# Optimization experiments

Hardware: AMD Instinct MI355X
Metric: run time of the kernel (lower is better)

## Reference

```python
import jax, jax.numpy as jnp
import numpy as np

NUM_HEADS = 16
HEAD_DIM = 64
HIDDEN = NUM_HEADS * HEAD_DIM  # 1024
B, T = 32, 512


def setup_inputs() -> dict:
    key = jax.random.key(0)
    ks = jax.random.split(key, 10)
    s = 1.0 / np.sqrt(HIDDEN)
    inp = {
        "x": jax.random.normal(ks[0], (B, HIDDEN, T), dtype=jnp.float32),
        "mask": jax.random.randint(ks[1], (B, T), 0, 2, dtype=jnp.int32),
        "Wq": jax.random.uniform(ks[2], (HIDDEN, HIDDEN), jnp.float32, -s, s),
        "bq": jax.random.uniform(ks[3], (HIDDEN,), jnp.float32, -s, s),
        "Wk": jax.random.uniform(ks[4], (HIDDEN, HIDDEN), jnp.float32, -s, s),
        "bk": jax.random.uniform(ks[5], (HIDDEN,), jnp.float32, -s, s),
        "Wv": jax.random.uniform(ks[6], (HIDDEN, HIDDEN), jnp.float32, -s, s),
        "bv": jax.random.uniform(ks[7], (HIDDEN,), jnp.float32, -s, s),
        "Wo": jax.random.uniform(ks[8], (HIDDEN, HIDDEN), jnp.float32, -s, s),
        "bo": jax.random.uniform(ks[9], (HIDDEN,), jnp.float32, -s, s),
    }
    return inp


def reference(x, mask, Wq, bq, Wk, bk, Wv, bv, Wo, bo):
    # x: [B, hidden, T] -> tokens along last axis
    b, h, t = x.shape
    xt = jnp.swapaxes(x, 1, 2)  # [B, T, hidden]

    def heads(w, bias):
        y = xt @ w.T + bias                       # [B, T, hidden]
        return y.reshape(b, t, NUM_HEADS, HEAD_DIM).transpose(0, 2, 1, 3)  # [B, nh, T, hd]

    q = heads(Wq, bq)
    k = heads(Wk, bk)
    v = heads(Wv, bv)

    scores = jnp.einsum("bhqd,bhkd->bhqk", q, k) / jnp.sqrt(jnp.float32(HEAD_DIM))
    # masked_fill(mask==0, -inf) then clamp to [-50, 50]: masked entries become -50
    scores = jnp.where(mask[:, None, None, :] == 0, -jnp.inf, scores)
    scores = jnp.clip(scores, -50.0, 50.0)
    attn = jax.nn.softmax(scores, axis=-1)        # [B, nh, T, T]
    out = jnp.einsum("bhqk,bhkd->bhqd", attn, v)  # [B, nh, T, hd]
    out = out.transpose(0, 2, 1, 3).reshape(b, t, h)
    out = out @ Wo.T + bo                         # [B, T, hidden]
    return out.max(axis=1)                        # [B, hidden]
```

## Files before the change

kernel.cpp:

```cpp
#include <hip/hip_runtime.h>


typedef _Float16 half8 __attribute__((ext_vector_type(8)));
typedef _Float16 half4 __attribute__((ext_vector_type(4)));
typedef float floatx4 __attribute__((ext_vector_type(4)));
typedef unsigned uintx2 __attribute__((ext_vector_type(2)));

#define HID 1024
#define TT 512
#define NB 32
#define QSCALE 0.1803368801111244f
#define SB2 72.13475204444817f

__device__ __forceinline__ void gload16(const void* g, void* l) {
    __builtin_amdgcn_global_load_lds(
        (const __attribute__((address_space(1))) unsigned int*)g,
        (__attribute__((address_space(3))) unsigned int*)l, 16, 0, 0);
}

__device__ __forceinline__ unsigned fkey(float f) {
    unsigned u = __float_as_uint(f);
    return (u & 0x80000000u) ? ~u : (u | 0x80000000u);
}
__device__ __forceinline__ float funkey(unsigned k) {
    unsigned u = (k & 0x80000000u) ? (k ^ 0x80000000u) : ~k;
    return __uint_as_float(u);
}

__global__ __launch_bounds__(256) void prep_kernel(
    const float* __restrict__ Wq, const float* __restrict__ Wk,
    const float* __restrict__ Wv, const float* __restrict__ Wo,
    _Float16* __restrict__ Wcat,
    const float* __restrict__ x, _Float16* __restrict__ xT,
    unsigned* __restrict__ omax,
    const float* __restrict__ bq, float* __restrict__ bqs)
{
    __shared__ float tile[64][65];
    const int bid = blockIdx.x;
    if (bid < 4096) {
        int i4 = bid * 256 + threadIdx.x;
        int sec = i4 >> 18;
        int off4 = i4 & ((1 << 18) - 1);
        const float* src = (sec == 0) ? Wq : (sec == 1) ? Wk
                          : (sec == 2) ? Wv : Wo;
        float4 v = ((const float4*)src)[off4];
        if (sec == 0) {
            v.x *= QSCALE; v.y *= QSCALE; v.z *= QSCALE; v.w *= QSCALE;
        }
        half4 h = {(_Float16)v.x, (_Float16)v.y, (_Float16)v.z, (_Float16)v.w};
        *(half4*)(Wcat + (size_t)i4 * 4) = h;
    } else if (bid < 8192) {
        int idx = bid - 4096;
        int b = idx >> 7, h0 = ((idx >> 3) & 15) * 64, t0 = (idx & 7) * 64;
        int tx = threadIdx.x & 15, ty = threadIdx.x >> 4;
        const float* xb = x + ((size_t)b * HID + h0) * TT + t0;
        for (int p = 0; p < 4; p++) {
            int r = ty + 16 * p;
            float4 v = *(const float4*)(xb + (size_t)r * TT + tx * 4);
            tile[r][tx * 4 + 0] = v.x;
            tile[r][tx * 4 + 1] = v.y;
            tile[r][tx * 4 + 2] = v.z;
            tile[r][tx * 4 + 3] = v.w;
        }
        __syncthreads();
        int hc = (threadIdx.x & 7) * 8, tb = threadIdx.x >> 3;
        for (int rd = 0; rd < 2; rd++) {
            int tt = tb + 32 * rd;
            half8 pk;
            for (int k = 0; k < 8; k++)
                pk[k] = (_Float16)tile[hc + k][tt];
            *(half8*)(xT + ((size_t)b * TT + t0 + tt) * HID + h0 + hc) = pk;
        }
    } else if (bid < 8320) {
        omax[(bid - 8192) * 256 + threadIdx.x] = 0u;
    } else {
        int i = (bid - 8320) * 256 + threadIdx.x;
        bqs[i] = bq[i] * QSCALE;
    }
}

#define PH_PRE do { \
    __builtin_amdgcn_s_barrier(); \
    asm volatile("s_waitcnt lgkmcnt(0)" ::: "memory"); \
    __builtin_amdgcn_sched_barrier(0); \
    __builtin_amdgcn_s_setprio(1); \
} while (0)

#define PH_POST(N) do { \
    __builtin_amdgcn_s_setprio(0); \
    asm volatile("s_waitcnt vmcnt(" #N ")" ::: "memory"); \
    __builtin_amdgcn_s_barrier(); \
} while (0)

#define LDA(P, MH) do { \
    const _Float16* ab_ = lds + (P) * 16384 + (MH) * 8192 + aoff; \
    af[0][0] = *(const half8*)(ab_ + pb0); \
    af[0][1] = *(const half8*)(ab_ + pb1); \
    af[1][0] = *(const half8*)(ab_ + 1024 + pb0); \
    af[1][1] = *(const half8*)(ab_ + 1024 + pb1); \
    af[2][0] = *(const half8*)(ab_ + 2048 + pb0); \
    af[2][1] = *(const half8*)(ab_ + 2048 + pb1); \
    af[3][0] = *(const half8*)(ab_ + 3072 + pb0); \
    af[3][1] = *(const half8*)(ab_ + 3072 + pb1); \
} while (0)

#define LDB(P, NH) do { \
    const _Float16* bb_ = lds + 32768 + (P) * 16384 + (NH) * 8192 + boff; \
    bf[NH][0][0] = *(const half8*)(bb_ + pb0); \
    bf[NH][0][1] = *(const half8*)(bb_ + pb1); \
    bf[NH][1][0] = *(const half8*)(bb_ + 1024 + pb0); \
    bf[NH][1][1] = *(const half8*)(bb_ + 1024 + pb1); \
} while (0)

#define MFMAQ(MH, NH) do { \
    _Pragma("unroll") \
    for (int j_ = 0; j_ < 4; ++j_) { \
        _Pragma("unroll") \
        for (int n_ = 0; n_ < 2; ++n_) { \
            floatx4 c_ = acc[(MH) * 4 + j_][(NH) * 2 + n_]; \
            c_ = __builtin_amdgcn_mfma_f32_16x16x32_f16( \
                af[j_][0], bf[NH][n_][0], c_, 0, 0, 0); \
            c_ = __builtin_amdgcn_mfma_f32_16x16x32_f16( \
                af[j_][1], bf[NH][n_][1], c_, 0, 0, 0); \
            acc[(MH) * 4 + j_][(NH) * 2 + n_] = c_; \
        } \
    } \
} while (0)

#define STAGE_A(P, MH, K0) do { \
    _Float16* d_ = lds + (P) * 16384 + (MH) * 8192 + wst; \
    gload16(ag + (MH) * 65536 + (K0), d_); \
    gload16(ag + 131072 + (MH) * 65536 + (K0), d_ + 4096); \
} while (0)

#define STAGE_B(P, NH, K0) do { \
    _Float16* d_ = lds + 32768 + (P) * 16384 + (NH) * 8192 + wst; \
    gload16(bg + (NH) * 32768 + (K0), d_); \
    gload16(bg + 131072 + (NH) * 32768 + (K0), d_ + 4096); \
} while (0)

__device__ __forceinline__ void mainloop256(
    const _Float16* __restrict__ Ag,
    const _Float16* __restrict__ Bg,
    _Float16* lds, floatx4 acc[8][4], int tid)
{
    const int lane = tid & 63;
    const int w = tid >> 6, wr = w >> 2, wc = w & 3;
    const int l15 = lane & 15, quad = lane >> 4;
    const int pa = quad ^ (l15 & 7);
    const int pb0 = pa * 8, pb1 = (pa ^ 4) * 8;
    const int aoff = (wr * 64 + l15) * 64;
    const int boff = (wc * 32 + l15) * 64;
    const int wst = w * 512;
    const int r = tid >> 3;
    const int sg = (tid & 7) ^ (r & 7);
    const int nbase = ((r >> 5) << 6) + (r & 31);
    const _Float16* ag = Ag + (size_t)r * 1024 + sg * 8;
    const _Float16* bg = Bg + (size_t)nbase * 1024 + sg * 8;

    half8 af[4][2], bf[2][2][2];

    STAGE_A(0, 0, 0); STAGE_B(0, 0, 0); STAGE_B(0, 1, 0); STAGE_A(0, 1, 0);
    STAGE_A(1, 0, 64); STAGE_B(1, 0, 64); STAGE_B(1, 1, 64);
    asm volatile("s_waitcnt vmcnt(10)" ::: "memory");
    __builtin_amdgcn_s_barrier();

    for (int i = 0; i < 7; ++i) {
        const int kb = i * 128 + 64;
        const int kn0 = kb + 64, kn1 = kb + 128;
        LDA(0, 0); LDB(0, 0); STAGE_A(1, 1, kb);
        PH_PRE; MFMAQ(0, 0); PH_POST(10);
        LDB(0, 1);            STAGE_A(0, 0, kn0);
        PH_PRE; MFMAQ(0, 1); PH_POST(10);
        LDA(0, 1);            STAGE_B(0, 0, kn0);
        PH_PRE; MFMAQ(1, 1); PH_POST(10);
                              STAGE_B(0, 1, kn0);
        PH_PRE; MFMAQ(1, 0); PH_POST(10);
        LDA(1, 0); LDB(1, 0); STAGE_A(0, 1, kn0);
        PH_PRE; MFMAQ(0, 0); PH_POST(10);
        LDB(1, 1);            STAGE_A(1, 0, kn1);
        PH_PRE; MFMAQ(0, 1); PH_POST(10);
        LDA(1, 1);            STAGE_B(1, 0, kn1);
        PH_PRE; MFMAQ(1, 1); PH_POST(10);
                              STAGE_B(1, 1, kn1);
        PH_PRE; MFMAQ(1, 0); PH_POST(10);
    }
    LDA(0, 0); LDB(0, 0); STAGE_A(1, 1, 960);
    PH_PRE; MFMAQ(0, 0); PH_POST(10);
    LDB(0, 1);
    PH_PRE; MFMAQ(0, 1); PH_POST(8);
    LDA(0, 1);
    PH_PRE; MFMAQ(1, 1); PH_POST(6);
    PH_PRE; MFMAQ(1, 0); PH_POST(4);
    LDA(1, 0); LDB(1, 0);
    PH_PRE; MFMAQ(0, 0); PH_POST(2);
    LDB(1, 1);
    PH_PRE; MFMAQ(0, 1); PH_POST(0);
    LDA(1, 1);
    PH_PRE; MFMAQ(1, 1); MFMAQ(1, 0);
    __builtin_amdgcn_s_setprio(0);
}

__global__ __launch_bounds__(512, 2) void gemm1_kernel(
    const _Float16* __restrict__ Wcat,
    const float* __restrict__ bqs, const float* __restrict__ bk,
    const float* __restrict__ bv,
    const _Float16* __restrict__ xT,
    _Float16* __restrict__ QT, _Float16* __restrict__ KT,
    _Float16* __restrict__ Vb)
{
    __shared__ __align__(16) _Float16 smem[65536];
    const int tid = threadIdx.x;
    const int id = blockIdx.x;
    const int xcd = id & 7, slot = id >> 3;
    const int grp = xcd + 8 * (slot / 12);
    const int m0 = (slot % 12) * 256;
    const int n0 = (grp & 1) * 256;
    const int bb = grp >> 1;
    const int lane = tid & 63;
    const int w = tid >> 6, wr = w >> 2, wc = w & 3;
    const int l15 = lane & 15, quad = lane >> 4;

    floatx4 acc[8][4] = {};
    mainloop256(Wcat + (size_t)m0 * 1024,
                xT + ((size_t)bb * TT + n0) * HID, smem, acc, tid);
    __syncthreads();

    const int sec = m0 >> 10;
    const int mo = m0 & 1023;

    if (sec < 2) {
        const float* bias = (sec == 0) ? bqs : bk;
        _Float16* dst = (sec == 0) ? QT : KT;
        _Float16* tr = smem;
        for (int h = 0; h < 2; ++h) {
            if (wr == h) {
                for (int mi = 0; mi < 8; ++mi) {
                    float bs[4];
                    for (int rr = 0; rr < 4; ++rr)
                        bs[rr] = bias[mo + h * 128 + mi * 16 + quad * 4 + rr];
                    for (int ni = 0; ni < 4; ++ni) {
                        half4 pk;
                        for (int rr = 0; rr < 4; ++rr)
                            pk[rr] = (_Float16)(acc[mi][ni][rr] + bs[rr]);
                        *(half4*)(tr + (wc * 64 + ni * 16 + l15) * 136 +
                                  mi * 16 + quad * 4) = pk;
                    }
                }
            }
            __syncthreads();
            const int row = tid >> 4, off = (tid & 15) * 8;
            for (int s = 0; s < 8; ++s) {
                uint4 v = *(uint4*)(tr + (row + 32 * s) * 136 + off);
                *(uint4*)(dst + ((size_t)bb * TT + n0 + row + 32 * s) * HID +
                          mo + h * 128 + off) = v;
            }
            __syncthreads();
        }
    } else {
        for (int mi = 0; mi < 8; ++mi) {
            float bs[4];
            for (int rr = 0; rr < 4; ++rr)
                bs[rr] = bv[mo + wr * 128 + mi * 16 + quad * 4 + rr];
            for (int ni = 0; ni < 4; ++ni) {
                int t = n0 + wc * 64 + ni * 16 + l15;
                for (int rr = 0; rr < 4; ++rr) {
                    int o = mo + wr * 128 + mi * 16 + quad * 4 + rr;
                    Vb[((size_t)bb * HID + o) * TT + t] =
                        (_Float16)(acc[mi][ni][rr] + bs[rr]);
                }
            }
        }
    }
}

__global__ __launch_bounds__(512, 4) void attn_kernel(
    const _Float16* __restrict__ QT, const _Float16* __restrict__ KT,
    const _Float16* __restrict__ Vb, const int* __restrict__ mask,
    _Float16* __restrict__ OcT)
{
    __shared__ __align__(16) _Float16 kvbuf[4 * 4096];
    __shared__ __align__(16) _Float16 ps[2 * 8192];
    __shared__ __align__(16) float msf[2][64];

    const int id = blockIdx.x;
    const int xcd = id & 7, slot = id >> 3;
    const int grp = xcd + 8 * (slot >> 1);
    const int q0 = (slot & 1) * 256;
    const int hd = grp & 15, b = grp >> 4;
    const int tid = threadIdx.x;
    const int lane = tid & 63, wid = tid >> 6;
    const int l15 = lane & 15, quad = lane >> 4;

    const _Float16* QTb = QT + ((size_t)b * TT + q0) * HID + hd * 64;
    const _Float16* KTb = KT + (size_t)b * TT * HID + hd * 64;
    const _Float16* Vbb = Vb + ((size_t)b * HID + hd * 64) * TT;
    const int* mb = mask + b * TT;

    const int srow = lane >> 3;
    const int sg = (lane & 7) ^ srow;
    const int pa = quad ^ (l15 & 7);
    const int pz = l15 & 7;

    for (int p = 0; p < 4; p++) {
        int r = p * 64 + wid * 8 + srow;
        gload16(QTb + (size_t)r * HID + sg * 8,
                kvbuf + (p * 64 + wid * 8) * 64);
    }
    __syncthreads();
    half8 bq[2][2];
    for (int qt = 0; qt < 2; qt++) {
        int qr = qt * 128 + wid * 16 + l15;
        bq[qt][0] = *(half8*)(kvbuf + qr * 64 + pa * 8);
        bq[qt][1] = *(half8*)(kvbuf + qr * 64 + (pa ^ 4) * 8);
    }
    __syncthreads();

    auto stage = [&](int jcn, int bufn) {
        int t0n = jcn * 64;
        _Float16* kd = kvbuf + bufn * 4096;
        _Float16* vd = kvbuf + (2 + bufn) * 4096;
        int r = wid * 8 + srow;
        gload16(KTb + (size_t)(t0n + r) * HID + sg * 8, kd + (wid * 8) * 64);
        gload16(Vbb + (size_t)r * TT + t0n + sg * 8, vd + (wid * 8) * 64);
        if (tid < 64) msf[bufn][tid] = mb[t0n + tid] ? SB2 : -SB2;
    };

    stage(0, 0);

    floatx4 oacc[2][4] = {};
    float rs[2] = {0.f, 0.f};
    const float lo = -SB2;

    for (int jc = 0; jc < 8; jc++) {
        const int cur = jc & 1;
        __syncthreads();
        if (jc < 7) stage(jc + 1, 1 - cur);

        const _Float16* ks = kvbuf + cur * 4096;
        const _Float16* vs = kvbuf + (2 + cur) * 4096;

        for (int jt = 0; jt < 4; jt++) {
            half8 ka0 = *(half8*)(ks + (jt * 16 + l15) * 64 + pa * 8);
            half8 ka1 = *(half8*)(ks + (jt * 16 + l15) * 64 + (pa ^ 4) * 8);
            floatx4 hi = *(floatx4*)(&msf[cur][jt * 16 + quad * 4]);
            for (int qt = 0; qt < 2; qt++) {
                floatx4 sc = {0.f, 0.f, 0.f, 0.f};
                sc = __builtin_amdgcn_mfma_f32_16x16x32_f16(ka0, bq[qt][0], sc, 0, 0, 0);
                sc = __builtin_amdgcn_mfma_f32_16x16x32_f16(ka1, bq[qt][1], sc, 0, 0, 0);
                float e0 = __builtin_amdgcn_exp2f(fminf(fmaxf(sc[0], lo), hi[0]));
                float e1 = __builtin_amdgcn_exp2f(fminf(fmaxf(sc[1], lo), hi[1]));
                float e2 = __builtin_amdgcn_exp2f(fminf(fmaxf(sc[2], lo), hi[2]));
                float e3 = __builtin_amdgcn_exp2f(fminf(fmaxf(sc[3], lo), hi[3]));
                rs[qt] += (e0 + e1) + (e2 + e3);
                unsigned uA = __builtin_bit_cast(
                    unsigned, __builtin_amdgcn_cvt_pkrtz(e0, e1));
                unsigned uB = __builtin_bit_cast(
                    unsigned, __builtin_amdgcn_cvt_pkrtz(e2, e3));
                uintx2 uv = {uA, uB};
                half4 pk = __builtin_bit_cast(half4, uv);
                int g = jt * 2 + (quad >> 1);
                *(half4*)(ps + qt * 8192 + (wid * 16 + l15) * 64 + (g ^ pz) * 8 +
                          (quad & 1) * 4) = pk;
            }
        }
        for (int kc = 0; kc < 2; kc++) {
            int g = kc * 4 + quad;
            half8 bv8[4];
            for (int d4 = 0; d4 < 4; d4++)
                bv8[d4] = *(half8*)(vs + (d4 * 16 + l15) * 64 + (g ^ pz) * 8);
            for (int qt = 0; qt < 2; qt++) {
                half8 ap = *(half8*)(ps + qt * 8192 + (wid * 16 + l15) * 64 +
                                     (g ^ pz) * 8);
                for (int d4 = 0; d4 < 4; d4++)
                    oacc[qt][d4] = __builtin_amdgcn_mfma_f32_16x16x32_f16(
                        ap, bv8[d4], oacc[qt][d4], 0, 0, 0);
            }
        }
    }

    for (int qt = 0; qt < 2; qt++) {
        float s = rs[qt];
        s += __shfl_xor(s, 16, 64);
        s += __shfl_xor(s, 32, 64);
        s = 1.0f / s;
        float inv[4];
        for (int r = 0; r < 4; r++) inv[r] = __shfl(s, quad * 4 + r, 64);
        for (int d4 = 0; d4 < 4; d4++)
            for (int r = 0; r < 4; r++) {
                int t = q0 + qt * 128 + wid * 16 + quad * 4 + r;
                int c = hd * 64 + d4 * 16 + l15;
                OcT[((size_t)b * TT + t) * HID + c] =
                    (_Float16)(oacc[qt][d4][r] * inv[r]);
            }
    }
}

__global__ __launch_bounds__(512, 2) void gemm2_kernel(
    const _Float16* __restrict__ Wo16, const _Float16* __restrict__ OcT,
    unsigned* __restrict__ omax)
{
    __shared__ __align__(16) _Float16 smem[65536];
    _Float16* lds = smem;
    const int tid = threadIdx.x;
    const int id = blockIdx.x;
    const int xcd = id & 7, slot = id >> 3;
    const int grp = xcd + 8 * (slot >> 2);
    const int m0 = (slot & 3) * 256;
    const int n0 = (grp & 1) * 256;
    const int bb = grp >> 1;
    const int lane = tid & 63;
    const int w = tid >> 6, wr = w >> 2;
    const int l15 = lane & 15, quad = lane >> 4;

    floatx4 acc[8][4] = {};
    mainloop256(Wo16 + (size_t)m0 * 1024,
                OcT + ((size_t)bb * TT + n0) * HID, lds, acc, tid);

    for (int mi = 0; mi < 8; ++mi)
        for (int rr = 0; rr < 4; ++rr) {
            float v = acc[mi][0][rr];
            v = fmaxf(v, acc[mi][1][rr]);
            v = fmaxf(v, acc[mi][2][rr]);
            v = fmaxf(v, acc[mi][3][rr]);
            for (int d = 1; d < 16; d <<= 1)
                v = fmaxf(v, __shfl_xor(v, d, 64));
            if (l15 == 0) {
                int o = m0 + wr * 128 + mi * 16 + quad * 4 + rr;
                atomicMax(&omax[bb * HID + o], fkey(v));
            }
        }
}

__global__ __launch_bounds__(256) void final_kernel(
    const unsigned* __restrict__ omax, const float* __restrict__ bo,
    float* __restrict__ out)
{
    int i = blockIdx.x * 256 + threadIdx.x;
    out[i] = funkey(omax[i]) + bo[i & 1023];
}

extern "C" void kernel_launch(void* const* d_in, const int* in_sizes, int n_in,
                              void* d_out, int out_size, void* d_ws, size_t ws_size,
                              hipStream_t stream)
{
    const float* x  = (const float*)d_in[0];
    const int* mask = (const int*)d_in[1];
    const float* Wq = (const float*)d_in[2];
    const float* bq = (const float*)d_in[3];
    const float* Wk = (const float*)d_in[4];
    const float* bk = (const float*)d_in[5];
    const float* Wv = (const float*)d_in[6];
    const float* bv = (const float*)d_in[7];
    const float* Wo = (const float*)d_in[8];
    const float* bo = (const float*)d_in[9];
    float* out = (float*)d_out;

    char* ws = (char*)d_ws;
    _Float16* Wcat = (_Float16*)(ws);
    _Float16* xT   = (_Float16*)(ws + (8ull  << 20));
    _Float16* QT   = (_Float16*)(ws + (40ull << 20));
    _Float16* KT   = (_Float16*)(ws + (72ull << 20));
    _Float16* Vb   = (_Float16*)(ws + (104ull << 20));
    _Float16* OcT  = (_Float16*)(ws + (136ull << 20));
    unsigned* omax = (unsigned*)(ws + (168ull << 20));
    float*    bqs  = (float*)(ws + (168ull << 20) + (128ull << 10));

    prep_kernel<<<8324, 256, 0, stream>>>(Wq, Wk, Wv, Wo, Wcat, x, xT, omax,
                                          bq, bqs);
    gemm1_kernel<<<768, 512, 0, stream>>>(Wcat, bqs, bk, bv, xT, QT, KT, Vb);
    attn_kernel<<<1024, 512, 0, stream>>>(QT, KT, Vb, mask, OcT);
    gemm2_kernel<<<256, 512, 0, stream>>>(Wcat + (3ull << 20), OcT, omax);
    final_kernel<<<128, 256, 0, stream>>>(omax, bo, out);
}
```

Before: 321.6 us.

## Compact unmasked keys/values so attention iterates only over valid key tiles

Prep computes a per-batch prefix sum over the mask, giving each valid token a compacted index and a per-batch count, and zero-pads K/V up to the next 64-row tile. gemm1 scatters K and V rows to their compacted positions, dropping masked tokens. The attention loop then runs only ceil(count/64) key tiles and builds its mask from the count instead of reading the mask array. With a random mask about half the tiles are skipped. In exchange there are extra prep blocks, scattered stores in gemm1, and a data-dependent trip count.

```diff
diff --git a/kernel.cpp b/kernel.cpp
--- a/kernel.cpp
+++ b/kernel.cpp
@@ -33,7 +33,10 @@
     _Float16* __restrict__ Wcat,
     const float* __restrict__ x, _Float16* __restrict__ xT,
     unsigned* __restrict__ omax,
-    const float* __restrict__ bq, float* __restrict__ bqs)
+    const float* __restrict__ bq, float* __restrict__ bqs,
+    const int* __restrict__ mask, short* __restrict__ cp16,
+    int* __restrict__ Tcg, _Float16* __restrict__ KT,
+    _Float16* __restrict__ Vb)
 {
     __shared__ float tile[64][65];
     const int bid = blockIdx.x;
@@ -73,9 +76,43 @@
         }
     } else if (bid < 8320) {
         omax[(bid - 8192) * 256 + threadIdx.x] = 0u;
-    } else {
+    } else if (bid < 8324) {
         int i = (bid - 8320) * 256 + threadIdx.x;
         bqs[i] = bq[i] * QSCALE;
+    } else {
+        __shared__ int wsum[4];
+        __shared__ int tcs;
+        const int b = bid - 8324;
+        const int* mrow = mask + b * TT;
+        const int tid = threadIdx.x;
+        const int lane = tid & 63, wv = tid >> 6;
+        const int m0 = mrow[tid * 2] ? 1 : 0;
+        const int m1 = mrow[tid * 2 + 1] ? 1 : 0;
+        const int ps = m0 + m1;
+        int v = ps;
+        for (int d = 1; d < 64; d <<= 1) {
+            int u = __shfl_up(v, d, 64);
+            if (lane >= d) v += u;
+        }
+        if (lane == 63) wsum[wv] = v;
+        __syncthreads();
+        int off = 0;
+        for (int i = 0; i < 4; i++) off += (i < wv) ? wsum[i] : 0;
+        const int excl = off + v - ps;
+        cp16[(size_t)b * TT + tid * 2]     = m0 ? (short)excl : (short)-1;
+        cp16[(size_t)b * TT + tid * 2 + 1] = m1 ? (short)(excl + m0) : (short)-1;
+        if (tid == 255) { tcs = off + v; Tcg[b] = off + v; }
+        __syncthreads();
+        const int Tcv = tcs;
+        const int ce = (Tcv + 63) & ~63;
+        const int nrow = ce - Tcv;
+        half8 z8 = {};
+        _Float16* kb = KT + ((size_t)b * TT + Tcv) * HID;
+        for (int i = tid; i < nrow * 128; i += 256) ((half8*)kb)[i] = z8;
+        for (int o = tid; o < 1024; o += 256) {
+            _Float16* vr = Vb + ((size_t)b * HID + o) * TT;
+            for (int j = 0; j < nrow; j++) vr[Tcv + j] = (_Float16)0.f;
+        }
     }
 }
 
@@ -207,7 +244,7 @@
     const float* __restrict__ bv,
     const _Float16* __restrict__ xT,
     _Float16* __restrict__ QT, _Float16* __restrict__ KT,
-    _Float16* __restrict__ Vb)
+    _Float16* __restrict__ Vb, const short* __restrict__ cp16)
 {
     __shared__ __align__(16) _Float16 smem[65536];
     const int tid = threadIdx.x;
@@ -252,21 +289,31 @@
             const int row = tid >> 4, off = (tid & 15) * 8;
             for (int s = 0; s < 8; ++s) {
                 uint4 v = *(uint4*)(tr + (row + 32 * s) * 136 + off);
-                *(uint4*)(dst + ((size_t)bb * TT + n0 + row + 32 * s) * HID +
-                          mo + h * 128 + off) = v;
+                if (sec == 0) {
+                    *(uint4*)(dst + ((size_t)bb * TT + n0 + row + 32 * s) * HID +
+                              mo + h * 128 + off) = v;
+                } else {
+                    short cp = cp16[bb * TT + n0 + row + 32 * s];
+                    if (cp >= 0)
+                        *(uint4*)(dst + ((size_t)bb * TT + cp) * HID +
+                                  mo + h * 128 + off) = v;
+                }
             }
             __syncthreads();
         }
     } else {
+        short cps[4];
+        for (int ni = 0; ni < 4; ++ni)
+            cps[ni] = cp16[bb * TT + n0 + wc * 64 + ni * 16 + l15];
         for (int mi = 0; mi < 8; ++mi) {
             float bs[4];
             for (int rr = 0; rr < 4; ++rr)
                 bs[rr] = bv[mo + wr * 128 + mi * 16 + quad * 4 + rr];
             for (int ni = 0; ni < 4; ++ni) {
-                int t = n0 + wc * 64 + ni * 16 + l15;
+                if (cps[ni] < 0) continue;
                 for (int rr = 0; rr < 4; ++rr) {
                     int o = mo + wr * 128 + mi * 16 + quad * 4 + rr;
-                    Vb[((size_t)bb * HID + o) * TT + t] =
+                    Vb[((size_t)bb * HID + o) * TT + cps[ni]] =
                         (_Float16)(acc[mi][ni][rr] + bs[rr]);
                 }
             }
@@ -276,7 +323,7 @@
 
 __global__ __launch_bounds__(512, 4) void attn_kernel(
     const _Float16* __restrict__ QT, const _Float16* __restrict__ KT,
-    const _Float16* __restrict__ Vb, const int* __restrict__ mask,
+    const _Float16* __restrict__ Vb, const int* __restrict__ Tcg,
     _Float16* __restrict__ OcT)
 {
     __shared__ __align__(16) _Float16 kvbuf[4 * 4096];
@@ -295,7 +342,8 @@
     const _Float16* QTb = QT + ((size_t)b * TT + q0) * HID + hd * 64;
     const _Float16* KTb = KT + (size_t)b * TT * HID + hd * 64;
     const _Float16* Vbb = Vb + ((size_t)b * HID + hd * 64) * TT;
-    const int* mb = mask + b * TT;
+    const int Tc = Tcg[b];
+    const int nt = (Tc + 63) >> 6;
 
     const int srow = lane >> 3;
     const int sg = (lane & 7) ^ srow;
@@ -323,7 +371,7 @@
         int r = wid * 8 + srow;
         gload16(KTb + (size_t)(t0n + r) * HID + sg * 8, kd + (wid * 8) * 64);
         gload16(Vbb + (size_t)r * TT + t0n + sg * 8, vd + (wid * 8) * 64);
-        if (tid < 64) msf[bufn][tid] = mb[t0n + tid] ? SB2 : -SB2;
+        if (tid < 64) msf[bufn][tid] = (t0n + tid < Tc) ? SB2 : -SB2;
     };
 
     stage(0, 0);
@@ -332,10 +380,10 @@
     float rs[2] = {0.f, 0.f};
     const float lo = -SB2;
 
-    for (int jc = 0; jc < 8; jc++) {
+    for (int jc = 0; jc < nt; jc++) {
         const int cur = jc & 1;
         __syncthreads();
-        if (jc < 7) stage(jc + 1, 1 - cur);
+        if (jc < nt - 1) stage(jc + 1, 1 - cur);
 
         const _Float16* ks = kvbuf + cur * 4096;
         const _Float16* vs = kvbuf + (2 + cur) * 4096;
@@ -465,11 +513,14 @@
     _Float16* OcT  = (_Float16*)(ws + (136ull << 20));
     unsigned* omax = (unsigned*)(ws + (168ull << 20));
     float*    bqs  = (float*)(ws + (168ull << 20) + (128ull << 10));
-
-    prep_kernel<<<8324, 256, 0, stream>>>(Wq, Wk, Wv, Wo, Wcat, x, xT, omax,
-                                          bq, bqs);
-    gemm1_kernel<<<768, 512, 0, stream>>>(Wcat, bqs, bk, bv, xT, QT, KT, Vb);
-    attn_kernel<<<1024, 512, 0, stream>>>(QT, KT, Vb, mask, OcT);
+    short*    cp16 = (short*)(ws + (168ull << 20) + (132ull << 10));
+    int*      Tcg  = (int*)  (ws + (168ull << 20) + (164ull << 10));
+
+    prep_kernel<<<8356, 256, 0, stream>>>(Wq, Wk, Wv, Wo, Wcat, x, xT, omax,
+                                          bq, bqs, mask, cp16, Tcg, KT, Vb);
+    gemm1_kernel<<<768, 512, 0, stream>>>(Wcat, bqs, bk, bv, xT, QT, KT, Vb,
+                                          cp16);
+    attn_kernel<<<1024, 512, 0, stream>>>(QT, KT, Vb, Tcg, OcT);
     gemm2_kernel<<<256, 512, 0, stream>>>(Wcat + (3ull << 20), OcT, omax);
     final_kernel<<<128, 256, 0, stream>>>(omax, bo, out);
 }
```

Measured after the change: 320.2 us. No clear change (-0.4%).
